# Performance work log

Measured on AMD Instinct MI355X. Metric: run time of the kernel, lower is better.

The kernel has to match this reference:

```python
import jax, jax.numpy as jnp
import numpy as np


def setup_inputs() -> dict:
    key = jax.random.key(0)
    k1, k2, k3 = jax.random.split(key, 3)
    B, N, D, T = 8, 2, 256, 500
    SPK = 2000
    H = jax.random.normal(k1, (B, N, D, T), dtype=jnp.float32)
    S = jax.random.randint(k2, (B, N, T), 0, SPK, dtype=jnp.int64)
    E = jax.random.normal(k3, (SPK, D), dtype=jnp.float32)
    alpha = jnp.ones((1,), dtype=jnp.float32) * 10.0
    beta = jnp.ones((1,), dtype=jnp.float32) * 5.0
    return {"H": H, "S": S, "E": E, "alpha": alpha, "beta": beta, "N": 2}


def reference(H, S, E, alpha, beta, N):
    # H: (B, N, D, T); S: (B, N, T) int ids; E: (SPK, D)
    B, N_, D, T = H.shape
    # embedding lookup: (B, N, T, D) -> (B, N, D, T)
    E_S = jnp.transpose(E[S], (0, 1, 3, 2))
    # pairwise dist between predicted vectors and active-speaker embeddings
    # (B, N_pred=N, N_emb=N, T) -- small, direct broadcast
    Dist_p = jnp.sum((H[:, None, :, :, :] - E_S[:, :, None, :, :]) ** 2, axis=3)
    # N == 2 path matching (identity vs swap), min over the two alignments
    p0 = Dist_p[:, 0, 0, :] + Dist_p[:, 1, 1, :]  # (B, T)
    p1 = Dist_p[:, 0, 1, :] + Dist_p[:, 1, 0, :]  # (B, T)
    Dmin = jnp.minimum(p0, p1)                    # (B, T)
    Dmin = -alpha * Dmin + beta                   # broadcast (1,) over (B, T)
    # full distance to every speaker: ||H||^2 + ||E||^2 - 2 H.E
    # avoids materializing (B, SPK, N, D, T)
    Hsq = jnp.sum(H * H, axis=2)                  # (B, N, T)
    Esq = jnp.sum(E * E, axis=1)                  # (SPK,)
    cross = jnp.einsum('bndt,sd->bsnt', H, E)     # (B, SPK, N, T)
    Dist = Hsq[:, None, :, :] + Esq[None, :, None, None] - 2.0 * cross
    Dist = -alpha * Dist + beta                   # (B, SPK, N, T)
    lse = jax.nn.logsumexp(Dist, axis=1)          # (B, N, T)
    loss = -jnp.mean(Dmin) + jnp.mean(lse)
    return (E_S[:, :, :, 0], loss)
```

## Files before the change

### kernel.cpp

```cpp
#include <hip/hip_runtime.h>
#include <math.h>

#define Bb   8
#define Dd   256
#define Tt   500
#define SPK  2000
#define SPKP 2048
#define BN   16
#define L2E  1.4426950408889634f
#define LN2  0.6931471805599453f

#define EXP2F(x) __builtin_amdgcn_exp2f(x)
#define LOG2F(x) __builtin_amdgcn_logf(x)

#define F_ESN   0
#define F_HSQP  4096
#define F_PM    36864
#define F_PL    69632
#define F_DMP2  102400
#define EBF_BYTES ((size_t)167936 * 4)
#define HBF_BYTES (EBF_BYTES + (size_t)1048576)

#define ROWSTRIDE 264

typedef __bf16 v8bf __attribute__((ext_vector_type(8)));
typedef float  v4f  __attribute__((ext_vector_type(4)));

__device__ inline unsigned pack_bf16x2(float lo, float hi) {
    union { __bf16 h; unsigned short u; } a, b;
    a.h = (__bf16)lo; b.h = (__bf16)hi;
    return ((unsigned)b.u << 16) | (unsigned)a.u;
}

__global__ __launch_bounds__(256) void prep_all_kernel(
        const float* __restrict__ E, const int* __restrict__ S,
        const float* __restrict__ H, const float* __restrict__ alpha,
        const float* __restrict__ beta, float* __restrict__ ws,
        float* __restrict__ out) {
    int bid = blockIdx.x;
    int tid = threadIdx.x;

    if (bid < 512) {
        int s = bid * 4 + (tid >> 6);
        int lane = tid & 63;
        float4 v = make_float4(0.f, 0.f, 0.f, 0.f);
        if (s < SPK) v = ((const float4*)E)[s * 64 + lane];
        __bf16* ebf = (__bf16*)((char*)ws + EBF_BYTES);
        uint2 pp;
        pp.x = pack_bf16x2(v.x, v.y);
        pp.y = pack_bf16x2(v.z, v.w);
        *(uint2*)(ebf + (size_t)s * Dd + lane * 4) = pp;
        float acc = v.x * v.x + v.y * v.y + v.z * v.z + v.w * v.w;
        #pragma unroll
        for (int off = 32; off > 0; off >>= 1) acc += __shfl_down(acc, off, 64);
        if (lane == 0) ws[F_ESN + s] = (s < SPK) ? (-alpha[0] * acc * L2E) : -1e30f;
    } else if (bid < 528) {
        if (bid == 512 && tid == 0) out[BN * Dd] = 0.f;
        int i = (bid - 512) * 256 + tid;
        int bn = i >> 8, d = i & 255;
        out[i] = E[(size_t)S[bn * Tt] * Dd + d];
    } else {
        __shared__ float trans[32][65];
        int u = bid - 528;
        int bn = u >> 6;
        int r = u & 63;
        int tt0 = (r & 15) * 32;
        int d0 = (r >> 4) * 64;
        const float* Hb = H + (size_t)bn * Dd * Tt;
        #pragma unroll
        for (int p = 0; p < 8; ++p) {
            int flat = p * 256 + tid;
            int dd = flat >> 5;
            int tl = flat & 31;
            int t = tt0 + tl;
            trans[tl][dd] = (t < Tt) ? Hb[(size_t)(d0 + dd) * Tt + t] : 0.f;
        }
        __syncthreads();
        int tw = tid >> 3;
        int j = tid & 7;
        int t = tt0 + tw;
        bool ok = (t < Tt);
        int tc = ok ? t : (Tt - 1);
        int b = bn >> 1;
        int s0 = S[(b * 2 + 0) * Tt + tc];
        int s1 = S[(b * 2 + 1) * Tt + tc];
        const float4* e0p = (const float4*)(E + (size_t)s0 * Dd + d0 + j * 8);
        const float4* e1p = (const float4*)(E + (size_t)s1 * Dd + d0 + j * 8);
        float4 ea0 = e0p[0], ea1 = e0p[1];
        float4 eb0 = e1p[0], eb1 = e1p[1];
        float ev0[8] = {ea0.x, ea0.y, ea0.z, ea0.w, ea1.x, ea1.y, ea1.z, ea1.w};
        float ev1[8] = {eb0.x, eb0.y, eb0.z, eb0.w, eb1.x, eb1.y, eb1.z, eb1.w};
        float sq = 0.f, p0 = 0.f, p1 = 0.f;
        float vals[8];
        #pragma unroll
        for (int e = 0; e < 8; ++e) {
            float x = trans[tw][j * 8 + e];
            vals[e] = x;
            sq = fmaf(x, x, sq);
            float u0 = x - ev0[e]; p0 = fmaf(u0, u0, p0);
            float u1 = x - ev1[e]; p1 = fmaf(u1, u1, p1);
        }
        sq += __shfl_xor(sq, 1, 64); p0 += __shfl_xor(p0, 1, 64); p1 += __shfl_xor(p1, 1, 64);
        sq += __shfl_xor(sq, 2, 64); p0 += __shfl_xor(p0, 2, 64); p1 += __shfl_xor(p1, 2, 64);
        sq += __shfl_xor(sq, 4, 64); p0 += __shfl_xor(p0, 4, 64); p1 += __shfl_xor(p1, 4, 64);
        uint4 pk;
        pk.x = pack_bf16x2(vals[0], vals[1]);
        pk.y = pack_bf16x2(vals[2], vals[3]);
        pk.z = pack_bf16x2(vals[4], vals[5]);
        pk.w = pack_bf16x2(vals[6], vals[7]);
        __bf16* hbf = (__bf16*)((char*)ws + HBF_BYTES);
        *(uint4*)(hbf + ((size_t)(bn * 512 + t) * Dd + d0 + j * 8)) = pk;
        if (j == 0) {
            ws[F_HSQP + (size_t)(bn * 512 + t) * 4 + (r >> 4)] = sq;
            if (ok) {
                float2 pr = make_float2(p0, p1);
                *(float2*)(ws + F_DMP2 + (((size_t)bn * 512 + t) * 4 + (r >> 4)) * 2) = pr;
            }
        }
    }
}

__global__ __launch_bounds__(256, 2) void lse_mfma_kernel(
        const float* __restrict__ alpha, const float* __restrict__ beta,
        float* __restrict__ ws) {
    __shared__ __bf16 shB[64 * ROWSTRIDE];
    __shared__ __bf16 shA[64 * ROWSTRIDE];
    __shared__ float mrg_m[4][4][16], mrg_l[4][4][16];

    int bn = blockIdx.x;
    int t0 = blockIdx.y * 64;
    int mz = blockIdx.z;
    int tid = threadIdx.x;
    int lane = tid & 63;
    int n = lane & 15;
    int q = lane >> 4;
    int w = tid >> 6;

    const __bf16* ebf = (const __bf16*)((const char*)ws + EBF_BYTES);
    const __bf16* hbf = (const __bf16*)((const char*)ws + HBF_BYTES);

    #pragma unroll
    for (int p = 0; p < 8; ++p) {
        int flat = p * 256 + tid;
        int row = flat >> 5;
        int ch = flat & 31;
        uint4 vb = *(const uint4*)(hbf + ((size_t)(bn * 512 + t0 + row) * Dd + ch * 8));
        *(uint4*)(shB + row * ROWSTRIDE + ch * 8) = vb;
    }

    __bf16* shAw = shA + w * (16 * ROWSTRIDE);
    __bf16* shBw = shB + w * (16 * ROWSTRIDE);

    {
        int sbase = mz * 512 + w * 16;
        uint4 t0r[8];
        #pragma unroll
        for (int p = 0; p < 8; ++p) {
            int flat = p * 64 + lane, row = flat >> 5, ch = flat & 31;
            t0r[p] = *(const uint4*)(ebf + ((size_t)(sbase + row) * Dd + ch * 8));
        }
        #pragma unroll
        for (int p = 0; p < 8; ++p) {
            int flat = p * 64 + lane, row = flat >> 5, ch = flat & 31;
            *(uint4*)(shAw + row * ROWSTRIDE + ch * 8) = t0r[p];
        }
    }

    __syncthreads();

    v8bf bq[4][8];
    #pragma unroll
    for (int i = 0; i < 4; ++i) {
        int tloc = 16 * i + n;
        #pragma unroll
        for (int ks = 0; ks < 8; ++ks) {
            bq[i][ks] = *reinterpret_cast<const v8bf*>(&shB[tloc * ROWSTRIDE + ks * 32 + q * 8]);
        }
    }
    __syncthreads();

    float A = alpha[0], Bv = beta[0];
    float ta2p = 2.f * A * L2E;
    float ctc2[4];
    #pragma unroll
    for (int i = 0; i < 4; ++i) {
        int t = t0 + 16 * i + n;
        float4 hq = *(const float4*)(ws + F_HSQP + (size_t)(bn * 512 + t) * 4);
        float hs = hq.x + hq.y + hq.z + hq.w;
        ctc2[i] = (t < Tt) ? ((Bv - A * hs) * L2E) : 0.f;
    }

    float lm[4], ll[4];
    #pragma unroll
    for (int i = 0; i < 4; ++i) { lm[i] = -INFINITY; ll[i] = 0.f; }

    auto chunk = [&](const __bf16* curw, __bf16* nxtw, int c, bool last) {
        int sbase = mz * 512 + c * 64 + w * 16;
        uint4 tmp[8];
        if (!last) {
            int nb = sbase + 64;
            #pragma unroll
            for (int p = 0; p < 8; ++p) {
                int flat = p * 64 + lane, row = flat >> 5, ch = flat & 31;
                tmp[p] = *(const uint4*)(ebf + ((size_t)(nb + row) * Dd + ch * 8));
            }
        }

        v8bf af[8];
        #pragma unroll
        for (int ks = 0; ks < 8; ++ks) {
            af[ks] = *reinterpret_cast<const v8bf*>(&curw[n * ROWSTRIDE + ks * 32 + q * 8]);
        }
        float4 es4 = *(const float4*)(ws + F_ESN + sbase + q * 4);

        v4f acc[4];
        #pragma unroll
        for (int i = 0; i < 4; ++i) acc[i] = (v4f){0.f, 0.f, 0.f, 0.f};
        #pragma unroll
        for (int ks = 0; ks < 8; ++ks) {
            #pragma unroll
            for (int i = 0; i < 4; ++i) {
                acc[i] = __builtin_amdgcn_mfma_f32_16x16x32_bf16(af[ks], bq[i][ks], acc[i], 0, 0, 0);
            }
        }
        float e0 = es4.x, e1 = es4.y, e2 = es4.z, e3 = es4.w;
        #pragma unroll
        for (int i = 0; i < 4; ++i) {
            float c2 = ctc2[i];
            float v0 = fmaf(ta2p, acc[i][0], c2 + e0);
            float v1 = fmaf(ta2p, acc[i][1], c2 + e1);
            float v2 = fmaf(ta2p, acc[i][2], c2 + e2);
            float v3 = fmaf(ta2p, acc[i][3], c2 + e3);
            float vm = fmaxf(fmaxf(v0, v1), fmaxf(v2, v3));
            float s = EXP2F(v0 - vm) + EXP2F(v1 - vm) + EXP2F(v2 - vm) + EXP2F(v3 - vm);
            float nm = fmaxf(lm[i], vm);
            ll[i] = ll[i] * EXP2F(lm[i] - nm) + s * EXP2F(vm - nm);
            lm[i] = nm;
        }

        if (!last) {
            #pragma unroll
            for (int p = 0; p < 8; ++p) {
                int flat = p * 64 + lane, row = flat >> 5, ch = flat & 31;
                *(uint4*)(&nxtw[row * ROWSTRIDE + ch * 8]) = tmp[p];
            }
        }
    };

    for (int cc = 0; cc < 4; ++cc) {
        chunk(shAw, shBw, 2 * cc, false);
        chunk(shBw, shAw, 2 * cc + 1, cc == 3);
    }

    #pragma unroll
    for (int i = 0; i < 4; ++i) {
        float m = lm[i], l = ll[i];
        #pragma unroll
        for (int msk = 16; msk <= 32; msk <<= 1) {
            float om = __shfl_xor(m, msk, 64);
            float ol = __shfl_xor(l, msk, 64);
            float nm = fmaxf(m, om);
            l = l * EXP2F(m - nm) + ol * EXP2F(om - nm);
            m = nm;
        }
        if (q == 0) { mrg_m[w][i][n] = m; mrg_l[w][i][n] = l; }
    }
    __syncthreads();

    if (tid < 64) {
        int i = tid >> 4, cc = tid & 15;
        float m = mrg_m[0][i][cc], l = mrg_l[0][i][cc];
        #pragma unroll
        for (int wv = 1; wv < 4; ++wv) {
            float om = mrg_m[wv][i][cc], ol = mrg_l[wv][i][cc];
            float nm = fmaxf(m, om);
            l = l * EXP2F(m - nm) + ol * EXP2F(om - nm);
            m = nm;
        }
        int tw = t0 + 16 * i + cc;
        if (tw < Tt) {
            ws[F_PM + (bn * 512 + tw) * 4 + mz] = m;
            ws[F_PL + (bn * 512 + tw) * 4 + mz] = l;
        }
    }
}

__global__ __launch_bounds__(512) void final_kernel(
        const float* __restrict__ alpha, const float* __restrict__ beta,
        const float* __restrict__ ws, float* __restrict__ out) {
    __shared__ float rL[8], rD[8];
    int b = blockIdx.x;
    int tid = threadIdx.x;
    float A = alpha[0], Bv = beta[0];

    float lsum = 0.f, dsum = 0.f;
    int t = tid;
    if (t < Tt) {
        #pragma unroll
        for (int nn = 0; nn < 2; ++nn) {
            int idx = (b * 2 + nn) * 512 + t;
            float4 m4 = *(const float4*)(ws + F_PM + (size_t)idx * 4);
            float4 l4 = *(const float4*)(ws + F_PL + (size_t)idx * 4);
            float m = m4.x, l = l4.x, nm;
            nm = fmaxf(m, m4.y); l = l * EXP2F(m - nm) + l4.y * EXP2F(m4.y - nm); m = nm;
            nm = fmaxf(m, m4.z); l = l * EXP2F(m - nm) + l4.z * EXP2F(m4.z - nm); m = nm;
            nm = fmaxf(m, m4.w); l = l * EXP2F(m - nm) + l4.w * EXP2F(m4.w - nm); m = nm;
            lsum += LN2 * (m + LOG2F(l));
        }
        const float4* P0 = (const float4*)(ws + F_DMP2 + ((size_t)(2 * b + 0) * 512 + t) * 8);
        const float4* P1 = (const float4*)(ws + F_DMP2 + ((size_t)(2 * b + 1) * 512 + t) * 8);
        float4 a0 = P0[0], a1 = P0[1];
        float4 b0 = P1[0], b1 = P1[1];
        float d00 = a0.x + a0.z + a1.x + a1.z;
        float d01 = a0.y + a0.w + a1.y + a1.w;
        float d10 = b0.x + b0.z + b1.x + b1.z;
        float d11 = b0.y + b0.w + b1.y + b1.w;
        float dm = fminf(d00 + d11, d01 + d10);
        dsum = -A * dm + Bv;
    }

    int lane = tid & 63, w = tid >> 6;
    #pragma unroll
    for (int off = 32; off > 0; off >>= 1) {
        lsum += __shfl_down(lsum, off, 64);
        dsum += __shfl_down(dsum, off, 64);
    }
    if (lane == 0) { rL[w] = lsum; rD[w] = dsum; }
    __syncthreads();
    if (tid == 0) {
        float L = 0.f, D = 0.f;
        #pragma unroll
        for (int wv = 0; wv < 8; ++wv) { L += rL[wv]; D += rD[wv]; }
        atomicAdd(&out[BN * Dd], -(D / (float)(Bb * Tt)) + L / (float)(BN * Tt));
    }
}

extern "C" void kernel_launch(void* const* d_in, const int* in_sizes, int n_in,
                              void* d_out, int out_size, void* d_ws, size_t ws_size,
                              hipStream_t stream) {
    const float* H     = (const float*)d_in[0];
    const int*   S     = (const int*)d_in[1];
    const float* E     = (const float*)d_in[2];
    const float* alpha = (const float*)d_in[3];
    const float* beta  = (const float*)d_in[4];
    float* out = (float*)d_out;
    float* ws  = (float*)d_ws;

    prep_all_kernel<<<1552, 256, 0, stream>>>(E, S, H, alpha, beta, ws, out);
    lse_mfma_kernel<<<dim3(BN, 8, 4), 256, 0, stream>>>(alpha, beta, ws);
    final_kernel<<<8, 512, 0, stream>>>(alpha, beta, ws, out);
}
```

Baseline: 113.5 us.

## Fuse H transpose and bf16 conversion into LSE kernel, shrink prep stage

Removes the prep-stage H transpose that wrote bf16 H and partial squared norms to the workspace. The LSE MFMA kernel now reads fp32 H directly, transposes it through shared memory, converts it to bf16 and computes the squared norms itself. The Dmin path in prep is rewritten to compute all four pair distances per timestep and reduce them to one partial sum per block, so the final kernel only sums 16 values per batch. The E double-buffer prefetch is dropped in favour of a simpler per-chunk load. This trades a workspace round trip for redundant H reads, since four mz blocks each transpose the same H tile, and for lost load/compute overlap.

```diff
diff --git a/kernel.cpp b/kernel.cpp
--- a/kernel.cpp
+++ b/kernel.cpp
@@ -14,12 +14,10 @@
 #define LOG2F(x) __builtin_amdgcn_logf(x)
 
 #define F_ESN   0
-#define F_HSQP  4096
+#define F_DMINP 2048
 #define F_PM    36864
 #define F_PL    69632
-#define F_DMP2  102400
 #define EBF_BYTES ((size_t)167936 * 4)
-#define HBF_BYTES (EBF_BYTES + (size_t)1048576)
 
 #define ROWSTRIDE 264
 
@@ -60,71 +58,59 @@
         int bn = i >> 8, d = i & 255;
         out[i] = E[(size_t)S[bn * Tt] * Dd + d];
     } else {
-        __shared__ float trans[32][65];
-        int u = bid - 528;
-        int bn = u >> 6;
-        int r = u & 63;
-        int tt0 = (r & 15) * 32;
-        int d0 = (r >> 4) * 64;
-        const float* Hb = H + (size_t)bn * Dd * Tt;
-        #pragma unroll
-        for (int p = 0; p < 8; ++p) {
-            int flat = p * 256 + tid;
-            int dd = flat >> 5;
-            int tl = flat & 31;
-            int t = tt0 + tl;
-            trans[tl][dd] = (t < Tt) ? Hb[(size_t)(d0 + dd) * Tt + t] : 0.f;
-        }
-        __syncthreads();
-        int tw = tid >> 3;
-        int j = tid & 7;
-        int t = tt0 + tw;
+        __shared__ float4 shm[8][32];
+        int qq = bid - 528;
+        int b = qq >> 4;
+        int t0 = (qq & 15) * 32;
+        int tl = tid & 31;
+        int wv = tid >> 5;
+        int t = t0 + tl;
         bool ok = (t < Tt);
         int tc = ok ? t : (Tt - 1);
-        int b = bn >> 1;
         int s0 = S[(b * 2 + 0) * Tt + tc];
         int s1 = S[(b * 2 + 1) * Tt + tc];
-        const float4* e0p = (const float4*)(E + (size_t)s0 * Dd + d0 + j * 8);
-        const float4* e1p = (const float4*)(E + (size_t)s1 * Dd + d0 + j * 8);
-        float4 ea0 = e0p[0], ea1 = e0p[1];
-        float4 eb0 = e1p[0], eb1 = e1p[1];
-        float ev0[8] = {ea0.x, ea0.y, ea0.z, ea0.w, ea1.x, ea1.y, ea1.z, ea1.w};
-        float ev1[8] = {eb0.x, eb0.y, eb0.z, eb0.w, eb1.x, eb1.y, eb1.z, eb1.w};
-        float sq = 0.f, p0 = 0.f, p1 = 0.f;
-        float vals[8];
-        #pragma unroll
-        for (int e = 0; e < 8; ++e) {
-            float x = trans[tw][j * 8 + e];
-            vals[e] = x;
-            sq = fmaf(x, x, sq);
-            float u0 = x - ev0[e]; p0 = fmaf(u0, u0, p0);
-            float u1 = x - ev1[e]; p1 = fmaf(u1, u1, p1);
-        }
-        sq += __shfl_xor(sq, 1, 64); p0 += __shfl_xor(p0, 1, 64); p1 += __shfl_xor(p1, 1, 64);
-        sq += __shfl_xor(sq, 2, 64); p0 += __shfl_xor(p0, 2, 64); p1 += __shfl_xor(p1, 2, 64);
-        sq += __shfl_xor(sq, 4, 64); p0 += __shfl_xor(p0, 4, 64); p1 += __shfl_xor(p1, 4, 64);
-        uint4 pk;
-        pk.x = pack_bf16x2(vals[0], vals[1]);
-        pk.y = pack_bf16x2(vals[2], vals[3]);
-        pk.z = pack_bf16x2(vals[4], vals[5]);
-        pk.w = pack_bf16x2(vals[6], vals[7]);
-        __bf16* hbf = (__bf16*)((char*)ws + HBF_BYTES);
-        *(uint4*)(hbf + ((size_t)(bn * 512 + t) * Dd + d0 + j * 8)) = pk;
-        if (j == 0) {
-            ws[F_HSQP + (size_t)(bn * 512 + t) * 4 + (r >> 4)] = sq;
-            if (ok) {
-                float2 pr = make_float2(p0, p1);
-                *(float2*)(ws + F_DMP2 + (((size_t)bn * 512 + t) * 4 + (r >> 4)) * 2) = pr;
-            }
+        const float* h0 = H + ((size_t)(b * 2 + 0) * Dd) * Tt + tc;
+        const float* h1 = H + ((size_t)(b * 2 + 1) * Dd) * Tt + tc;
+        const float* e0 = E + (size_t)s0 * Dd;
+        const float* e1 = E + (size_t)s1 * Dd;
+        float d00 = 0, d01 = 0, d10 = 0, d11 = 0;
+        int dbase = wv * 32;
+        #pragma unroll 4
+        for (int dd = 0; dd < 32; ++dd) {
+            int d = dbase + dd;
+            float x0 = h0[(size_t)d * Tt], x1 = h1[(size_t)d * Tt];
+            float y0 = e0[d], y1 = e1[d];
+            float u;
+            u = x0 - y0; d00 = fmaf(u, u, d00);
+            u = x0 - y1; d01 = fmaf(u, u, d01);
+            u = x1 - y0; d10 = fmaf(u, u, d10);
+            u = x1 - y1; d11 = fmaf(u, u, d11);
+        }
+        shm[wv][tl] = make_float4(d00, d01, d10, d11);
+        __syncthreads();
+        if (tid < 32) {
+            d00 = 0; d01 = 0; d10 = 0; d11 = 0;
+            #pragma unroll
+            for (int g = 0; g < 8; ++g) {
+                float4 p = shm[g][tl];
+                d00 += p.x; d01 += p.y; d10 += p.z; d11 += p.w;
+            }
+            float dm = fminf(d00 + d11, d01 + d10);
+            float val = ok ? (-alpha[0] * dm + beta[0]) : 0.f;
+            #pragma unroll
+            for (int off = 16; off > 0; off >>= 1) val += __shfl_down(val, off, 32);
+            if (tid == 0) ws[F_DMINP + qq] = val;
         }
     }
 }
 
 __global__ __launch_bounds__(256, 2) void lse_mfma_kernel(
-        const float* __restrict__ alpha, const float* __restrict__ beta,
-        float* __restrict__ ws) {
+        const float* __restrict__ H, const float* __restrict__ alpha,
+        const float* __restrict__ beta, float* __restrict__ ws) {
     __shared__ __bf16 shB[64 * ROWSTRIDE];
     __shared__ __bf16 shA[64 * ROWSTRIDE];
+    __shared__ float trans[32][65];
+    __shared__ float hsqs[64];
     __shared__ float mrg_m[4][4][16], mrg_l[4][4][16];
 
     int bn = blockIdx.x;
@@ -137,19 +123,48 @@
     int w = tid >> 6;
 
     const __bf16* ebf = (const __bf16*)((const char*)ws + EBF_BYTES);
-    const __bf16* hbf = (const __bf16*)((const char*)ws + HBF_BYTES);
-
-    #pragma unroll
-    for (int p = 0; p < 8; ++p) {
-        int flat = p * 256 + tid;
-        int row = flat >> 5;
-        int ch = flat & 31;
-        uint4 vb = *(const uint4*)(hbf + ((size_t)(bn * 512 + t0 + row) * Dd + ch * 8));
-        *(uint4*)(shB + row * ROWSTRIDE + ch * 8) = vb;
+    const float* Hb = H + (size_t)bn * Dd * Tt;
+
+    {
+        int tw = tid >> 3;
+        int j = tid & 7;
+        #pragma unroll
+        for (int h = 0; h < 2; ++h) {
+            float sqacc = 0.f;
+            #pragma unroll
+            for (int dc = 0; dc < 4; ++dc) {
+                #pragma unroll
+                for (int p = 0; p < 8; ++p) {
+                    int flat = p * 256 + tid;
+                    int dd = flat >> 5;
+                    int tl = flat & 31;
+                    int t = t0 + h * 32 + tl;
+                    trans[tl][dd] = (t < Tt) ? Hb[(size_t)(dc * 64 + dd) * Tt + t] : 0.f;
+                }
+                __syncthreads();
+                float vals[8];
+                #pragma unroll
+                for (int e = 0; e < 8; ++e) {
+                    float x = trans[tw][j * 8 + e];
+                    vals[e] = x;
+                    sqacc = fmaf(x, x, sqacc);
+                }
+                uint4 pk;
+                pk.x = pack_bf16x2(vals[0], vals[1]);
+                pk.y = pack_bf16x2(vals[2], vals[3]);
+                pk.z = pack_bf16x2(vals[4], vals[5]);
+                pk.w = pack_bf16x2(vals[6], vals[7]);
+                *(uint4*)(&shB[(h * 32 + tw) * ROWSTRIDE + dc * 64 + j * 8]) = pk;
+                __syncthreads();
+            }
+            sqacc += __shfl_xor(sqacc, 1, 64);
+            sqacc += __shfl_xor(sqacc, 2, 64);
+            sqacc += __shfl_xor(sqacc, 4, 64);
+            if (j == 0) hsqs[h * 32 + tw] = sqacc;
+        }
     }
 
     __bf16* shAw = shA + w * (16 * ROWSTRIDE);
-    __bf16* shBw = shB + w * (16 * ROWSTRIDE);
 
     {
         int sbase = mz * 512 + w * 16;
@@ -177,7 +192,6 @@
             bq[i][ks] = *reinterpret_cast<const v8bf*>(&shB[tloc * ROWSTRIDE + ks * 32 + q * 8]);
         }
     }
-    __syncthreads();
 
     float A = alpha[0], Bv = beta[0];
     float ta2p = 2.f * A * L2E;
@@ -185,31 +199,35 @@
     #pragma unroll
     for (int i = 0; i < 4; ++i) {
         int t = t0 + 16 * i + n;
-        float4 hq = *(const float4*)(ws + F_HSQP + (size_t)(bn * 512 + t) * 4);
-        float hs = hq.x + hq.y + hq.z + hq.w;
-        ctc2[i] = (t < Tt) ? ((Bv - A * hs) * L2E) : 0.f;
+        ctc2[i] = (t < Tt) ? ((Bv - A * hsqs[16 * i + n]) * L2E) : 0.f;
     }
 
     float lm[4], ll[4];
     #pragma unroll
     for (int i = 0; i < 4; ++i) { lm[i] = -INFINITY; ll[i] = 0.f; }
 
-    auto chunk = [&](const __bf16* curw, __bf16* nxtw, int c, bool last) {
+    for (int c = 0; c < 8; ++c) {
         int sbase = mz * 512 + c * 64 + w * 16;
-        uint4 tmp[8];
-        if (!last) {
-            int nb = sbase + 64;
+
+        if (c > 0) {
+            uint4 tmp[8];
             #pragma unroll
             for (int p = 0; p < 8; ++p) {
                 int flat = p * 64 + lane, row = flat >> 5, ch = flat & 31;
-                tmp[p] = *(const uint4*)(ebf + ((size_t)(nb + row) * Dd + ch * 8));
-            }
-        }
+                tmp[p] = *(const uint4*)(ebf + ((size_t)(sbase + row) * Dd + ch * 8));
+            }
+            #pragma unroll
+            for (int p = 0; p < 8; ++p) {
+                int flat = p * 64 + lane, row = flat >> 5, ch = flat & 31;
+                *(uint4*)(shAw + row * ROWSTRIDE + ch * 8) = tmp[p];
+            }
+        }
+        __asm__ volatile("s_waitcnt lgkmcnt(0)" ::: "memory");
 
         v8bf af[8];
         #pragma unroll
         for (int ks = 0; ks < 8; ++ks) {
-            af[ks] = *reinterpret_cast<const v8bf*>(&curw[n * ROWSTRIDE + ks * 32 + q * 8]);
+            af[ks] = *reinterpret_cast<const v8bf*>(&shAw[n * ROWSTRIDE + ks * 32 + q * 8]);
         }
         float4 es4 = *(const float4*)(ws + F_ESN + sbase + q * 4);
 
@@ -237,19 +255,6 @@
             ll[i] = ll[i] * EXP2F(lm[i] - nm) + s * EXP2F(vm - nm);
             lm[i] = nm;
         }
-
-        if (!last) {
-            #pragma unroll
-            for (int p = 0; p < 8; ++p) {
-                int flat = p * 64 + lane, row = flat >> 5, ch = flat & 31;
-                *(uint4*)(&nxtw[row * ROWSTRIDE + ch * 8]) = tmp[p];
-            }
-        }
-    };
-
-    for (int cc = 0; cc < 4; ++cc) {
-        chunk(shAw, shBw, 2 * cc, false);
-        chunk(shBw, shAw, 2 * cc + 1, cc == 3);
     }
 
     #pragma unroll
@@ -291,9 +296,8 @@
     __shared__ float rL[8], rD[8];
     int b = blockIdx.x;
     int tid = threadIdx.x;
-    float A = alpha[0], Bv = beta[0];
-
-    float lsum = 0.f, dsum = 0.f;
+
+    float lsum = 0.f;
     int t = tid;
     if (t < Tt) {
         #pragma unroll
@@ -307,17 +311,8 @@
             nm = fmaxf(m, m4.w); l = l * EXP2F(m - nm) + l4.w * EXP2F(m4.w - nm); m = nm;
             lsum += LN2 * (m + LOG2F(l));
         }
-        const float4* P0 = (const float4*)(ws + F_DMP2 + ((size_t)(2 * b + 0) * 512 + t) * 8);
-        const float4* P1 = (const float4*)(ws + F_DMP2 + ((size_t)(2 * b + 1) * 512 + t) * 8);
-        float4 a0 = P0[0], a1 = P0[1];
-        float4 b0 = P1[0], b1 = P1[1];
-        float d00 = a0.x + a0.z + a1.x + a1.z;
-        float d01 = a0.y + a0.w + a1.y + a1.w;
-        float d10 = b0.x + b0.z + b1.x + b1.z;
-        float d11 = b0.y + b0.w + b1.y + b1.w;
-        float dm = fminf(d00 + d11, d01 + d10);
-        dsum = -A * dm + Bv;
-    }
+    }
+    float dsum = (tid < 16) ? ws[F_DMINP + b * 16 + tid] : 0.f;
 
     int lane = tid & 63, w = tid >> 6;
     #pragma unroll
@@ -346,7 +341,7 @@
     float* out = (float*)d_out;
     float* ws  = (float*)d_ws;
 
-    prep_all_kernel<<<1552, 256, 0, stream>>>(E, S, H, alpha, beta, ws, out);
-    lse_mfma_kernel<<<dim3(BN, 8, 4), 256, 0, stream>>>(alpha, beta, ws);
+    prep_all_kernel<<<656, 256, 0, stream>>>(E, S, H, alpha, beta, ws, out);
+    lse_mfma_kernel<<<dim3(BN, 8, 4), 256, 0, stream>>>(H, alpha, beta, ws);
     final_kernel<<<8, 512, 0, stream>>>(alpha, beta, ws, out);
 }
```

New measurement: 107.8 us. 5.0% less time.
